# Kernel optimization log

Hardware: AMD Instinct MI355X
Metric: run time of the kernel (lower is better)

Reference implementation:

```python
import jax, jax.numpy as jnp
import numpy as np

B, C, CI, H, W = 8, 256, 128, 64, 64
EPS = 1e-5

def conv1x1(x, w, b):
    # x: [B,C,H,W], w: [O,C], b: [O]
    return jnp.einsum('bchw,oc->bohw', x, w) + b[None, :, None, None]

def avgpool2(x):
    b, c, h, w = x.shape
    return x.reshape(b, c, h // 2, 2, w // 2, 2).mean(axis=(3, 5))

def setup_inputs() -> dict:
    key = jax.random.key(0)
    ks = jax.random.split(key, 16)
    s = lambda fan: 1.0 / np.sqrt(fan)
    inp = {
        'q': jax.random.normal(ks[0], (B, C, H, W), jnp.float32),
        'k': jax.random.normal(ks[1], (B, C, H, W), jnp.float32),
        'v': jax.random.normal(ks[2], (B, C, H, W), jnp.float32),
        'Wg':  jax.random.normal(ks[3], (CI, C), jnp.float32) * s(C),
        'bg':  jax.random.normal(ks[4], (CI,), jnp.float32) * s(C),
        'Wth': jax.random.normal(ks[5], (CI, C), jnp.float32) * s(C),
        'bth': jax.random.normal(ks[6], (CI,), jnp.float32) * s(C),
        'Wph': jax.random.normal(ks[7], (CI, C), jnp.float32) * s(C),
        'bph': jax.random.normal(ks[8], (CI,), jnp.float32) * s(C),
        'Ww':  jax.random.normal(ks[9], (C, CI), jnp.float32) * s(CI),
        'bw':  jax.random.normal(ks[10], (C,), jnp.float32) * s(CI),
        'gamma': jax.random.normal(ks[11], (C,), jnp.float32) * 0.1 + 1.0,
        'beta':  jax.random.normal(ks[12], (C,), jnp.float32) * 0.1,
        'mean':  jax.random.normal(ks[13], (C,), jnp.float32) * 0.1,
        'var':   jax.random.uniform(ks[14], (C,), jnp.float32, 0.5, 1.5),
    }
    return inp

def reference(q, k, v, Wg, bg, Wth, bth, Wph, bph, Ww, bw, gamma, beta, mean, var):
    b = q.shape[0]
    # g branch on v, phi branch on q: 1x1 conv then 2x2 avg-pool (sub_sample)
    g_x = avgpool2(conv1x1(v, Wg, bg)).reshape(b, CI, -1)            # [B,CI,M]
    g_x = g_x.transpose(0, 2, 1)                                      # [B,M,CI]
    theta_x = conv1x1(k, Wth, bth).reshape(b, CI, -1).transpose(0, 2, 1)  # [B,N,CI]
    phi_x = avgpool2(conv1x1(q, Wph, bph)).reshape(b, CI, -1)        # [B,CI,M]
    f = jnp.einsum('bnc,bcm->bnm', theta_x, phi_x)                   # [B,N,M]
    f_div_C = jax.nn.softmax(f, axis=-1)
    y = jnp.einsum('bnm,bmc->bnc', f_div_C, g_x)                     # [B,N,CI]
    y = y.transpose(0, 2, 1).reshape(b, CI, H, W)
    W_y = conv1x1(y, Ww, bw)
    # BatchNorm2d (inference form)
    W_y = (W_y - mean[None, :, None, None]) * (gamma[None, :, None, None]
            * jax.lax.rsqrt(var + EPS)[None, :, None, None]) + beta[None, :, None, None]
    return W_y + v
```

## Files before the change

kernel.cpp:

```cpp
#include <hip/hip_runtime.h>
#include <cstddef>

typedef unsigned short u16;
typedef unsigned int u32;
typedef __attribute__((ext_vector_type(8))) __bf16 bf16x8;
typedef __attribute__((ext_vector_type(4))) float f32x4;

constexpr int kB = 8, kC = 256, kCI = 128, kN = 4096, kM = 1024;
constexpr int kCH = 64, kNCH = kM / kCH;
constexpr float kEPS = 1e-5f;
constexpr float kLOG2E = 1.44269504088896f;

__device__ __forceinline__ u16 f2bf(float f) {
    u32 u = __float_as_uint(f);
    u32 r = (u + 0x7fffu + ((u >> 16) & 1u)) >> 16;
    return (u16)r;
}

__device__ __forceinline__ void gload_lds16(const u16* g, u16* l) {
    __builtin_amdgcn_global_load_lds(
        (const __attribute__((address_space(1))) void*)g,
        (__attribute__((address_space(3))) void*)l, 16, 0, 0);
}

__global__ __launch_bounds__(256) void prep_kernel(const float* __restrict__ Wth,
                                                   const float* __restrict__ bth,
                                                   const float* __restrict__ Wph,
                                                   const float* __restrict__ Wg,
                                                   const float* __restrict__ Ww,
                                                   const float* __restrict__ bw,
                                                   const float* __restrict__ gamma,
                                                   const float* __restrict__ beta,
                                                   const float* __restrict__ mean,
                                                   const float* __restrict__ var,
                                                   u16* __restrict__ Wthb,
                                                   u16* __restrict__ Wphb,
                                                   u16* __restrict__ Wgb,
                                                   u16* __restrict__ Wwsb,
                                                   float* __restrict__ bb,
                                                   float* __restrict__ bthl) {
    int idx = blockIdx.x * 256 + threadIdx.x;
    if (idx < 32768) {
        Wthb[idx] = f2bf(Wth[idx] * kLOG2E);
        if (idx < kCI) bthl[idx] = bth[idx] * kLOG2E;
    } else if (idx < 65536) {
        int j = idx - 32768; Wphb[j] = f2bf(Wph[j]);
    } else if (idx < 98304) {
        int j = idx - 65536; Wgb[j] = f2bf(Wg[j]);
    } else {
        int j = idx - 98304;
        int co = j >> 7;
        float sc = gamma[co] * rsqrtf(var[co] + kEPS);
        Wwsb[j] = f2bf(Ww[j] * sc);
        if ((j & 127) == 0) bb[co] = (bw[co] - mean[co]) * sc + beta[co];
    }
}

template <int POOL>
__device__ __forceinline__ void conv_body(const float* __restrict__ x,
                                          const u16* __restrict__ Wb,
                                          const float* __restrict__ bias,
                                          u16* __restrict__ out, int Mn,
                                          int cmajor, int b, int n0,
                                          u16* x_lds) {
    int t = threadIdx.x;
    int w = t >> 6, lane = t & 63, l15 = lane & 15, quad = lane >> 4;
    int px = t & 63, cb8 = t >> 6;

    for (int cc8 = 0; cc8 < 8; cc8++) {
        int cb = cb8 * 8 + cc8;
        int c0 = cb * 8;
        float f[8];
        if (POOL) {
            int p = n0 + px, ph_ = p >> 5, pw_ = p & 31;
#pragma unroll
            for (int j = 0; j < 8; j++) {
                const float* src = x + ((size_t)(b * kC + c0 + j) * 64
                                        + 2 * ph_) * 64 + 2 * pw_;
                float2 a = *(const float2*)src;
                float2 b2 = *(const float2*)(src + 64);
                f[j] = 0.25f * (a.x + a.y + b2.x + b2.y);
            }
        } else {
#pragma unroll
            for (int j = 0; j < 8; j++)
                f[j] = x[(size_t)(b * kC + c0 + j) * Mn + n0 + px];
        }
        uint4 pk;
        pk.x = (u32)f2bf(f[0]) | ((u32)f2bf(f[1]) << 16);
        pk.y = (u32)f2bf(f[2]) | ((u32)f2bf(f[3]) << 16);
        pk.z = (u32)f2bf(f[4]) | ((u32)f2bf(f[5]) << 16);
        pk.w = (u32)f2bf(f[6]) | ((u32)f2bf(f[7]) << 16);
        *(uint4*)&x_lds[px * 256 + ((cb ^ (px & 7)) * 8)] = pk;
    }
    __syncthreads();

    f32x4 acc[8];
#pragma unroll
    for (int i = 0; i < 8; i++) acc[i] = (f32x4){0.f, 0.f, 0.f, 0.f};

    int rpx = w * 16 + l15;
#pragma unroll
    for (int ks = 0; ks < 8; ks++) {
        bf16x8 xf = *(const bf16x8*)&x_lds[rpx * 256 +
                                           (((ks * 4 + quad) ^ (rpx & 7)) * 8)];
#pragma unroll
        for (int ct = 0; ct < 8; ct++) {
            bf16x8 wf = *(const bf16x8*)&Wb[(ct * 16 + l15) * kC + ks * 32 + quad * 8];
            if (cmajor)
                acc[ct] = __builtin_amdgcn_mfma_f32_16x16x32_bf16(xf, wf, acc[ct], 0, 0, 0);
            else
                acc[ct] = __builtin_amdgcn_mfma_f32_16x16x32_bf16(wf, xf, acc[ct], 0, 0, 0);
        }
    }

    if (cmajor == 0) {
        int opx = n0 + w * 16 + l15;
#pragma unroll
        for (int ct = 0; ct < 8; ct++) {
            int ci0 = ct * 16 + quad * 4;
            uint2 pk;
            pk.x = (u32)f2bf(acc[ct][0] + bias[ci0 + 0]) |
                   ((u32)f2bf(acc[ct][1] + bias[ci0 + 1]) << 16);
            pk.y = (u32)f2bf(acc[ct][2] + bias[ci0 + 2]) |
                   ((u32)f2bf(acc[ct][3] + bias[ci0 + 3]) << 16);
            *(uint2*)&out[(size_t)(b * Mn + opx) * kCI + ci0] = pk;
        }
    } else {
        int opx = n0 + w * 16 + quad * 4;
#pragma unroll
        for (int ct = 0; ct < 8; ct++) {
            int ci = ct * 16 + l15;
            float bs = bias[ci];
            uint2 pk;
            pk.x = (u32)f2bf(acc[ct][0] + bs) | ((u32)f2bf(acc[ct][1] + bs) << 16);
            pk.y = (u32)f2bf(acc[ct][2] + bs) | ((u32)f2bf(acc[ct][3] + bs) << 16);
            *(uint2*)&out[(size_t)(b * kCI + ci) * Mn + opx] = pk;
        }
    }
}

__global__ __launch_bounds__(256, 4) void convs_kernel(const float* __restrict__ q,
                                                       const float* __restrict__ k,
                                                       const float* __restrict__ v,
                                                       const u16* __restrict__ Wthb,
                                                       const u16* __restrict__ Wphb,
                                                       const u16* __restrict__ Wgb,
                                                       const float* __restrict__ bthl,
                                                       const float* __restrict__ bph,
                                                       const float* __restrict__ bg,
                                                       u16* __restrict__ theta,
                                                       u16* __restrict__ phi,
                                                       u16* __restrict__ g) {
    __shared__ __align__(16) u16 x_lds[64 * 256];
    int bx = blockIdx.x, b = blockIdx.y;
    if (bx < 64) {
        conv_body<0>(k, Wthb, bthl, theta, kN, 0, b, bx * 64, x_lds);
    } else {
        int z = (bx >= 80);
        int n0 = (z ? (bx - 80) : (bx - 64)) * 64;
        conv_body<1>(z ? v : q, z ? Wgb : Wphb, z ? bg : bph, z ? g : phi,
                     kM, z, b, n0, x_lds);
    }
}

__global__ __launch_bounds__(256) void attn_kernel(const u16* __restrict__ theta,
                                                   const u16* __restrict__ phi,
                                                   const u16* __restrict__ g,
                                                   const u16* __restrict__ Wws,
                                                   const float* __restrict__ bb,
                                                   const float* __restrict__ v,
                                                   float* __restrict__ out) {
    __shared__ __align__(16) u16 ph_lds[2][8192];
    __shared__ __align__(16) u16 g_lds[2][8192];
    __shared__ __align__(16) u16 p_lds[4096];

    int t = threadIdx.x, b = blockIdx.y, n0 = blockIdx.x * 64;
    int w = t >> 6, lane = t & 63, l15 = lane & 15, quad = lane >> 4;
    int sw = (l15 >> 1) & 3;

    bf16x8 thf[4];
    const u16* thB = theta + ((size_t)(b * kN) + n0 + w * 16 + l15) * kCI;
#pragma unroll
    for (int ks = 0; ks < 4; ks++)
        thf[ks] = *(const bf16x8*)&thB[ks * 32 + quad * 8];

    f32x4 oacc[8];
#pragma unroll
    for (int ct = 0; ct < 8; ct++) oacc[ct] = (f32x4){0.f, 0.f, 0.f, 0.f};
    float m_ = -1e30f, l_ = 0.f;

    const u16* phB = phi + (size_t)b * kM * kCI;
    const u16* gB  = g   + (size_t)b * kCI * kM;
    u16* pw = p_lds + w * 1024;

    auto STAGE = [&](int buf, int ch) {
        int c0 = ch * kCH;
#pragma unroll
        for (int i = 0; i < 4; i++) {
            int W = t + 256 * i;
            int ks = W >> 8, m = (W >> 2) & 63, sl = W & 3;
            int cb = (ks << 2) | (sl ^ ((m >> 1) & 3));
            gload_lds16(phB + (size_t)(c0 + m) * kCI + cb * 8,
                        &ph_lds[buf][(w * 64 + i * 256) * 8]);
        }
#pragma unroll
        for (int i = 0; i < 4; i++) {
            int W = t + 256 * i;
            int ks2 = W >> 9, ci = (W >> 2) & 127, sl = W & 3;
            int mb = (ks2 << 2) | (sl ^ ((ci >> 1) & 3));
            gload_lds16(gB + (size_t)ci * kM + c0 + mb * 8,
                        &g_lds[buf][(w * 64 + i * 256) * 8]);
        }
    };

    STAGE(0, 0);

    for (int ch = 0; ch < kNCH; ++ch) {
        asm volatile("s_waitcnt vmcnt(0)" ::: "memory");
        __syncthreads();
        if (ch + 1 < kNCH) STAGE((ch + 1) & 1, ch + 1);
        const u16* phb = ph_lds[ch & 1];
        const u16* glb = g_lds[ch & 1];

        f32x4 sacc[4];
#pragma unroll
        for (int mt = 0; mt < 4; mt++) sacc[mt] = (f32x4){0.f, 0.f, 0.f, 0.f};
#pragma unroll
        for (int ks = 0; ks < 4; ks++)
#pragma unroll
            for (int mt = 0; mt < 4; mt++) {
                bf16x8 a = *(const bf16x8*)&phb[ks * 2048 + (mt * 16 + l15) * 32 +
                                                ((quad ^ sw) * 8)];
                sacc[mt] = __builtin_amdgcn_mfma_f32_16x16x32_bf16(a, thf[ks], sacc[mt], 0, 0, 0);
            }

        float mc = -1e30f;
#pragma unroll
        for (int mt = 0; mt < 4; mt++)
#pragma unroll
            for (int r = 0; r < 4; r++) mc = fmaxf(mc, sacc[mt][r]);
        mc = fmaxf(mc, __shfl_xor(mc, 16, 64));
        mc = fmaxf(mc, __shfl_xor(mc, 32, 64));
        if (__any(mc > m_ + 8.0f)) {
            float mn = fmaxf(m_, mc);
            float al = exp2f(m_ - mn);
            m_ = mn;
            l_ *= al;
#pragma unroll
            for (int ct = 0; ct < 8; ct++)
#pragma unroll
                for (int r = 0; r < 4; r++) oacc[ct][r] *= al;
        }
        float rs = 0.f;
#pragma unroll
        for (int mt = 0; mt < 4; mt++)
#pragma unroll
            for (int r = 0; r < 4; r++) {
                float p = exp2f(sacc[mt][r] - m_);
                sacc[mt][r] = p;
                rs += p;
            }
        l_ += rs;

#pragma unroll
        for (int mt = 0; mt < 4; mt++)
#pragma unroll
            for (int h = 0; h < 2; h++) {
                u32 d = (u32)f2bf(sacc[mt][2 * h]) | ((u32)f2bf(sacc[mt][2 * h + 1]) << 16);
                int m = mt * 16 + quad * 4 + 2 * h;
                int frag = m >> 5;
                int kblk = ((m >> 3) & 3);
                int j = (quad & 1) * 4 + 2 * h;
                *(u32*)&pw[frag * 512 + l15 * 32 + ((kblk ^ sw) * 8) + j] = d;
            }

#pragma unroll
        for (int ks2 = 0; ks2 < 2; ks2++) {
            bf16x8 bfrag = *(const bf16x8*)&pw[ks2 * 512 + l15 * 32 + ((quad ^ sw) * 8)];
#pragma unroll
            for (int ct = 0; ct < 8; ct++) {
                bf16x8 a = *(const bf16x8*)&glb[ks2 * 4096 + (ct * 16 + l15) * 32 +
                                                ((quad ^ sw) * 8)];
                oacc[ct] = __builtin_amdgcn_mfma_f32_16x16x32_bf16(a, bfrag, oacc[ct], 0, 0, 0);
            }
        }
    }

    l_ += __shfl_xor(l_, 16, 64);
    l_ += __shfl_xor(l_, 32, 64);
    float inv = 1.0f / l_;

    __syncthreads();
    u16* y_lds = &ph_lds[0][0];
    int nrow = w * 16 + l15;
#pragma unroll
    for (int ct = 0; ct < 8; ct++) {
        uint2 pk;
        pk.x = (u32)f2bf(oacc[ct][0] * inv) | ((u32)f2bf(oacc[ct][1] * inv) << 16);
        pk.y = (u32)f2bf(oacc[ct][2] * inv) | ((u32)f2bf(oacc[ct][3] * inv) << 16);
        *(uint2*)&y_lds[nrow * 136 + ct * 16 + quad * 4] = pk;
    }
    __syncthreads();

    bf16x8 af[4];
#pragma unroll
    for (int ks = 0; ks < 4; ks++)
        af[ks] = *(const bf16x8*)&y_lds[nrow * 136 + ks * 32 + quad * 8];

#pragma unroll
    for (int ct = 0; ct < 16; ct++) {
        int co = ct * 16 + l15;
        f32x4 a = (f32x4){0.f, 0.f, 0.f, 0.f};
#pragma unroll
        for (int ks = 0; ks < 4; ks++) {
            bf16x8 bf = *(const bf16x8*)&Wws[(size_t)co * kCI + ks * 32 + quad * 8];
            a = __builtin_amdgcn_mfma_f32_16x16x32_bf16(af[ks], bf, a, 0, 0, 0);
        }
        float bbv = bb[co];
        size_t base = (size_t)(b * kC + co) * kN + n0 + w * 16 + quad * 4;
        float4 vv = *(const float4*)&v[base];
        float4 ov;
        ov.x = a[0] + bbv + vv.x;
        ov.y = a[1] + bbv + vv.y;
        ov.z = a[2] + bbv + vv.z;
        ov.w = a[3] + bbv + vv.w;
        *(float4*)&out[base] = ov;
    }
}

extern "C" void kernel_launch(void* const* d_in, const int* in_sizes, int n_in,
                              void* d_out, int out_size, void* d_ws, size_t ws_size,
                              hipStream_t stream) {
    (void)in_sizes; (void)n_in; (void)out_size; (void)ws_size;
    const float* q     = (const float*)d_in[0];
    const float* k     = (const float*)d_in[1];
    const float* v     = (const float*)d_in[2];
    const float* Wg    = (const float*)d_in[3];
    const float* bg    = (const float*)d_in[4];
    const float* Wth   = (const float*)d_in[5];
    const float* bth   = (const float*)d_in[6];
    const float* Wph   = (const float*)d_in[7];
    const float* bph   = (const float*)d_in[8];
    const float* Ww    = (const float*)d_in[9];
    const float* bw    = (const float*)d_in[10];
    const float* gamma = (const float*)d_in[11];
    const float* beta  = (const float*)d_in[12];
    const float* mean  = (const float*)d_in[13];
    const float* var   = (const float*)d_in[14];
    float* out = (float*)d_out;

    u16* wsu = (u16*)d_ws;
    u16*   theta = wsu;
    u16*   phi   = theta + 4194304;
    u16*   gbuf  = phi + 1048576;
    u16*   Wthb  = gbuf + 1048576;
    u16*   Wphb  = Wthb + 32768;
    u16*   Wgb   = Wphb + 32768;
    u16*   Wwsb  = Wgb + 32768;
    float* bbuf  = (float*)(Wwsb + 32768);
    float* bthl  = bbuf + 256;

    prep_kernel<<<dim3(512), 256, 0, stream>>>(Wth, bth, Wph, Wg, Ww, bw, gamma, beta,
                                               mean, var, Wthb, Wphb, Wgb, Wwsb,
                                               bbuf, bthl);
    convs_kernel<<<dim3(96, 8), 256, 0, stream>>>(q, k, v, Wthb, Wphb, Wgb,
                                                  bthl, bph, bg, theta, phi, gbuf);
    attn_kernel<<<dim3(64, 8), 256, 0, stream>>>(theta, phi, gbuf, Wwsb, bbuf, v, out);
}
```

Measured before the change: 225.2 us.

## Fuse theta conv into attention kernel and split phi/g conv into smaller blocks

The theta 1x1 conv on k now runs inside the attention kernel's prologue. Each block converts its 64 pixels of k to bf16 in LDS, runs the MFMAs, and keeps the theta fragments in registers, so the 8 MB theta workspace is never written to or read back from global memory. The pooled phi/g convs move to their own kernel with 32-pixel tiles and a half-channel split per wave, giving 512 blocks instead of the previous 256 for that work. The cost is a longer attention prologue that reuses the phi/g LDS buffers with extra syncs, so the theta conv no longer overlaps with the other convs across the whole GPU.

```diff
diff --git a/kernel.cpp b/kernel.cpp
--- a/kernel.cpp
+++ b/kernel.cpp
@@ -56,35 +56,38 @@
     }
 }
 
-template <int POOL>
-__device__ __forceinline__ void conv_body(const float* __restrict__ x,
-                                          const u16* __restrict__ Wb,
-                                          const float* __restrict__ bias,
-                                          u16* __restrict__ out, int Mn,
-                                          int cmajor, int b, int n0,
-                                          u16* x_lds) {
+__global__ __launch_bounds__(256, 4) void convpg_kernel(const float* __restrict__ q,
+                                                        const float* __restrict__ v,
+                                                        const u16* __restrict__ Wphb,
+                                                        const u16* __restrict__ Wgb,
+                                                        const float* __restrict__ bph,
+                                                        const float* __restrict__ bg,
+                                                        u16* __restrict__ phi,
+                                                        u16* __restrict__ g) {
+    __shared__ __align__(16) u16 x_lds[32 * 256];
+    int z = blockIdx.z, b = blockIdx.y, n0 = blockIdx.x * 32;
+    const float* x = z ? v : q;
+    const u16* Wb = z ? Wgb : Wphb;
+    const float* bias = z ? bg : bph;
+    u16* outp = z ? g : phi;
+
     int t = threadIdx.x;
     int w = t >> 6, lane = t & 63, l15 = lane & 15, quad = lane >> 4;
-    int px = t & 63, cb8 = t >> 6;
-
-    for (int cc8 = 0; cc8 < 8; cc8++) {
-        int cb = cb8 * 8 + cc8;
+
+    int px = t & 31, cgrp = t >> 5;
+    int p = n0 + px, ph_ = p >> 5, pw_ = p & 31;
+#pragma unroll
+    for (int cc = 0; cc < 4; cc++) {
+        int cb = cgrp * 4 + cc;
         int c0 = cb * 8;
         float f[8];
-        if (POOL) {
-            int p = n0 + px, ph_ = p >> 5, pw_ = p & 31;
-#pragma unroll
-            for (int j = 0; j < 8; j++) {
-                const float* src = x + ((size_t)(b * kC + c0 + j) * 64
-                                        + 2 * ph_) * 64 + 2 * pw_;
-                float2 a = *(const float2*)src;
-                float2 b2 = *(const float2*)(src + 64);
-                f[j] = 0.25f * (a.x + a.y + b2.x + b2.y);
-            }
-        } else {
-#pragma unroll
-            for (int j = 0; j < 8; j++)
-                f[j] = x[(size_t)(b * kC + c0 + j) * Mn + n0 + px];
+#pragma unroll
+        for (int j = 0; j < 8; j++) {
+            const float* src = x + ((size_t)(b * kC + c0 + j) * 64 + 2 * ph_) * 64
+                               + 2 * pw_;
+            float2 a = *(const float2*)src;
+            float2 b2 = *(const float2*)(src + 64);
+            f[j] = 0.25f * (a.x + a.y + b2.x + b2.y);
         }
         uint4 pk;
         pk.x = (u32)f2bf(f[0]) | ((u32)f2bf(f[1]) << 16);
@@ -95,76 +98,56 @@
     }
     __syncthreads();
 
-    f32x4 acc[8];
-#pragma unroll
-    for (int i = 0; i < 8; i++) acc[i] = (f32x4){0.f, 0.f, 0.f, 0.f};
-
-    int rpx = w * 16 + l15;
+    int px_h = w >> 1, ci_h = w & 1;
+    f32x4 acc[4];
+#pragma unroll
+    for (int i = 0; i < 4; i++) acc[i] = (f32x4){0.f, 0.f, 0.f, 0.f};
+
+    int rpx = px_h * 16 + l15;
 #pragma unroll
     for (int ks = 0; ks < 8; ks++) {
         bf16x8 xf = *(const bf16x8*)&x_lds[rpx * 256 +
                                            (((ks * 4 + quad) ^ (rpx & 7)) * 8)];
 #pragma unroll
-        for (int ct = 0; ct < 8; ct++) {
-            bf16x8 wf = *(const bf16x8*)&Wb[(ct * 16 + l15) * kC + ks * 32 + quad * 8];
-            if (cmajor)
+        for (int ct = 0; ct < 4; ct++) {
+            int ci = ci_h * 64 + ct * 16 + l15;
+            bf16x8 wf = *(const bf16x8*)&Wb[ci * kC + ks * 32 + quad * 8];
+            if (z)
                 acc[ct] = __builtin_amdgcn_mfma_f32_16x16x32_bf16(xf, wf, acc[ct], 0, 0, 0);
             else
                 acc[ct] = __builtin_amdgcn_mfma_f32_16x16x32_bf16(wf, xf, acc[ct], 0, 0, 0);
         }
     }
 
-    if (cmajor == 0) {
-        int opx = n0 + w * 16 + l15;
-#pragma unroll
-        for (int ct = 0; ct < 8; ct++) {
-            int ci0 = ct * 16 + quad * 4;
+    if (!z) {
+        int opx = n0 + px_h * 16 + l15;
+#pragma unroll
+        for (int ct = 0; ct < 4; ct++) {
+            int ci0 = ci_h * 64 + ct * 16 + quad * 4;
             uint2 pk;
             pk.x = (u32)f2bf(acc[ct][0] + bias[ci0 + 0]) |
                    ((u32)f2bf(acc[ct][1] + bias[ci0 + 1]) << 16);
             pk.y = (u32)f2bf(acc[ct][2] + bias[ci0 + 2]) |
                    ((u32)f2bf(acc[ct][3] + bias[ci0 + 3]) << 16);
-            *(uint2*)&out[(size_t)(b * Mn + opx) * kCI + ci0] = pk;
+            *(uint2*)&outp[(size_t)(b * kM + opx) * kCI + ci0] = pk;
         }
     } else {
-        int opx = n0 + w * 16 + quad * 4;
-#pragma unroll
-        for (int ct = 0; ct < 8; ct++) {
-            int ci = ct * 16 + l15;
+        int opx = n0 + px_h * 16 + quad * 4;
+#pragma unroll
+        for (int ct = 0; ct < 4; ct++) {
+            int ci = ci_h * 64 + ct * 16 + l15;
             float bs = bias[ci];
             uint2 pk;
             pk.x = (u32)f2bf(acc[ct][0] + bs) | ((u32)f2bf(acc[ct][1] + bs) << 16);
             pk.y = (u32)f2bf(acc[ct][2] + bs) | ((u32)f2bf(acc[ct][3] + bs) << 16);
-            *(uint2*)&out[(size_t)(b * kCI + ci) * Mn + opx] = pk;
-        }
-    }
-}
-
-__global__ __launch_bounds__(256, 4) void convs_kernel(const float* __restrict__ q,
-                                                       const float* __restrict__ k,
-                                                       const float* __restrict__ v,
-                                                       const u16* __restrict__ Wthb,
-                                                       const u16* __restrict__ Wphb,
-                                                       const u16* __restrict__ Wgb,
-                                                       const float* __restrict__ bthl,
-                                                       const float* __restrict__ bph,
-                                                       const float* __restrict__ bg,
-                                                       u16* __restrict__ theta,
-                                                       u16* __restrict__ phi,
-                                                       u16* __restrict__ g) {
-    __shared__ __align__(16) u16 x_lds[64 * 256];
-    int bx = blockIdx.x, b = blockIdx.y;
-    if (bx < 64) {
-        conv_body<0>(k, Wthb, bthl, theta, kN, 0, b, bx * 64, x_lds);
-    } else {
-        int z = (bx >= 80);
-        int n0 = (z ? (bx - 80) : (bx - 64)) * 64;
-        conv_body<1>(z ? v : q, z ? Wgb : Wphb, z ? bg : bph, z ? g : phi,
-                     kM, z, b, n0, x_lds);
-    }
-}
-
-__global__ __launch_bounds__(256) void attn_kernel(const u16* __restrict__ theta,
+            *(uint2*)&outp[(size_t)(b * kCI + ci) * kM + opx] = pk;
+        }
+    }
+}
+
+__global__ __launch_bounds__(256) void attn_kernel(const float* __restrict__ k,
+                                                   const u16* __restrict__ Wthb,
+                                                   const float* __restrict__ bthl,
                                                    const u16* __restrict__ phi,
                                                    const u16* __restrict__ g,
                                                    const u16* __restrict__ Wws,
@@ -180,10 +163,55 @@
     int sw = (l15 >> 1) & 3;
 
     bf16x8 thf[4];
-    const u16* thB = theta + ((size_t)(b * kN) + n0 + w * 16 + l15) * kCI;
-#pragma unroll
-    for (int ks = 0; ks < 4; ks++)
-        thf[ks] = *(const bf16x8*)&thB[ks * 32 + quad * 8];
+    {
+        u16* x_lds = &ph_lds[0][0];
+        u16* th_lds = &g_lds[0][0];
+        int px = t & 63, cb8 = t >> 6;
+        for (int cc8 = 0; cc8 < 8; cc8++) {
+            int cb = cb8 * 8 + cc8;
+            int c0 = cb * 8;
+            float f[8];
+#pragma unroll
+            for (int j = 0; j < 8; j++)
+                f[j] = k[(size_t)(b * kC + c0 + j) * kN + n0 + px];
+            uint4 pk;
+            pk.x = (u32)f2bf(f[0]) | ((u32)f2bf(f[1]) << 16);
+            pk.y = (u32)f2bf(f[2]) | ((u32)f2bf(f[3]) << 16);
+            pk.z = (u32)f2bf(f[4]) | ((u32)f2bf(f[5]) << 16);
+            pk.w = (u32)f2bf(f[6]) | ((u32)f2bf(f[7]) << 16);
+            *(uint4*)&x_lds[px * 256 + ((cb ^ (px & 7)) * 8)] = pk;
+        }
+        __syncthreads();
+
+        f32x4 acc[8];
+#pragma unroll
+        for (int i = 0; i < 8; i++) acc[i] = (f32x4){0.f, 0.f, 0.f, 0.f};
+        int rpx = w * 16 + l15;
+#pragma unroll
+        for (int ks = 0; ks < 8; ks++) {
+            bf16x8 xf = *(const bf16x8*)&x_lds[rpx * 256 +
+                                               (((ks * 4 + quad) ^ (rpx & 7)) * 8)];
+#pragma unroll
+            for (int ct = 0; ct < 8; ct++) {
+                bf16x8 wf = *(const bf16x8*)&Wthb[(ct * 16 + l15) * kC + ks * 32 + quad * 8];
+                acc[ct] = __builtin_amdgcn_mfma_f32_16x16x32_bf16(wf, xf, acc[ct], 0, 0, 0);
+            }
+        }
+#pragma unroll
+        for (int ct = 0; ct < 8; ct++) {
+            int ci0 = ct * 16 + quad * 4;
+            uint2 pk;
+            pk.x = (u32)f2bf(acc[ct][0] + bthl[ci0 + 0]) |
+                   ((u32)f2bf(acc[ct][1] + bthl[ci0 + 1]) << 16);
+            pk.y = (u32)f2bf(acc[ct][2] + bthl[ci0 + 2]) |
+                   ((u32)f2bf(acc[ct][3] + bthl[ci0 + 3]) << 16);
+            *(uint2*)&th_lds[rpx * 136 + ci0] = pk;
+        }
+#pragma unroll
+        for (int ks = 0; ks < 4; ks++)
+            thf[ks] = *(const bf16x8*)&th_lds[rpx * 136 + ks * 32 + quad * 8];
+        __syncthreads();
+    }
 
     f32x4 oacc[8];
 #pragma unroll
@@ -351,8 +379,7 @@
     float* out = (float*)d_out;
 
     u16* wsu = (u16*)d_ws;
-    u16*   theta = wsu;
-    u16*   phi   = theta + 4194304;
+    u16*   phi   = wsu;
     u16*   gbuf  = phi + 1048576;
     u16*   Wthb  = gbuf + 1048576;
     u16*   Wphb  = Wthb + 32768;
@@ -364,7 +391,8 @@
     prep_kernel<<<dim3(512), 256, 0, stream>>>(Wth, bth, Wph, Wg, Ww, bw, gamma, beta,
                                                mean, var, Wthb, Wphb, Wgb, Wwsb,
                                                bbuf, bthl);
-    convs_kernel<<<dim3(96, 8), 256, 0, stream>>>(q, k, v, Wthb, Wphb, Wgb,
-                                                  bthl, bph, bg, theta, phi, gbuf);
-    attn_kernel<<<dim3(64, 8), 256, 0, stream>>>(theta, phi, gbuf, Wwsb, bbuf, v, out);
-}
+    convpg_kernel<<<dim3(32, 8, 2), 256, 0, stream>>>(q, v, Wphb, Wgb, bph, bg,
+                                                      phi, gbuf);
+    attn_kernel<<<dim3(64, 8), 256, 0, stream>>>(k, Wthb, bthl, phi, gbuf,
+                                                 Wwsb, bbuf, v, out);
+}
```

Measured after the change: 232.8 us. 1.03x slower.

## Split attention key dimension across two wave groups and merge softmax states

Applied to the files above, without the earlier changes.

The attention block grows to 512 threads, and the two groups of four waves each process half of the 1024 keys with 32-key chunks. The partial accumulators and max/sum statistics are merged through LDS in a flash-decoding-style combine. The output projection is then split across the groups by output channel. This raises per-CU wave parallelism on a grid of only 512 blocks, at the cost of an extra LDS exchange, more barriers and smaller per-chunk MFMA batches.

```diff
diff --git a/kernel.cpp b/kernel.cpp
--- a/kernel.cpp
+++ b/kernel.cpp
@@ -7,7 +7,9 @@
 typedef __attribute__((ext_vector_type(4))) float f32x4;
 
 constexpr int kB = 8, kC = 256, kCI = 128, kN = 4096, kM = 1024;
-constexpr int kCH = 64, kNCH = kM / kCH;
+constexpr int kHM = 512;
+constexpr int kCH = 32;
+constexpr int kNCH = kHM / kCH;
 constexpr float kEPS = 1e-5f;
 constexpr float kLOG2E = 1.44269504088896f;
 
@@ -164,23 +166,25 @@
     }
 }
 
-__global__ __launch_bounds__(256) void attn_kernel(const u16* __restrict__ theta,
-                                                   const u16* __restrict__ phi,
-                                                   const u16* __restrict__ g,
-                                                   const u16* __restrict__ Wws,
-                                                   const float* __restrict__ bb,
-                                                   const float* __restrict__ v,
-                                                   float* __restrict__ out) {
-    __shared__ __align__(16) u16 ph_lds[2][8192];
-    __shared__ __align__(16) u16 g_lds[2][8192];
-    __shared__ __align__(16) u16 p_lds[4096];
+__global__ __launch_bounds__(512, 4) void attn_kernel(const u16* __restrict__ theta,
+                                                      const u16* __restrict__ phi,
+                                                      const u16* __restrict__ g,
+                                                      const u16* __restrict__ Wws,
+                                                      const float* __restrict__ bb,
+                                                      const float* __restrict__ v,
+                                                      float* __restrict__ out) {
+    __shared__ __align__(16) u16 ph_lds[2][2][4096];
+    __shared__ __align__(16) u16 g_lds[2][2][4096];
+    __shared__ __align__(16) u16 p_lds[8 * 512];
+    __shared__ float mlsh[128];
 
     int t = threadIdx.x, b = blockIdx.y, n0 = blockIdx.x * 64;
     int w = t >> 6, lane = t & 63, l15 = lane & 15, quad = lane >> 4;
+    int grp = w >> 2, wl = w & 3, th = t & 255;
     int sw = (l15 >> 1) & 3;
 
     bf16x8 thf[4];
-    const u16* thB = theta + ((size_t)(b * kN) + n0 + w * 16 + l15) * kCI;
+    const u16* thB = theta + ((size_t)(b * kN) + n0 + wl * 16 + l15) * kCI;
 #pragma unroll
     for (int ks = 0; ks < 4; ks++)
         thf[ks] = *(const bf16x8*)&thB[ks * 32 + quad * 8];
@@ -192,25 +196,25 @@
 
     const u16* phB = phi + (size_t)b * kM * kCI;
     const u16* gB  = g   + (size_t)b * kCI * kM;
-    u16* pw = p_lds + w * 1024;
+    u16* pw = p_lds + w * 512;
 
     auto STAGE = [&](int buf, int ch) {
-        int c0 = ch * kCH;
-#pragma unroll
-        for (int i = 0; i < 4; i++) {
-            int W = t + 256 * i;
-            int ks = W >> 8, m = (W >> 2) & 63, sl = W & 3;
+        int c0 = grp * kHM + ch * kCH;
+#pragma unroll
+        for (int i = 0; i < 2; i++) {
+            int W = th + 256 * i;
+            int ks = W >> 7, m = (W >> 2) & 31, sl = W & 3;
             int cb = (ks << 2) | (sl ^ ((m >> 1) & 3));
             gload_lds16(phB + (size_t)(c0 + m) * kCI + cb * 8,
-                        &ph_lds[buf][(w * 64 + i * 256) * 8]);
-        }
-#pragma unroll
-        for (int i = 0; i < 4; i++) {
-            int W = t + 256 * i;
-            int ks2 = W >> 9, ci = (W >> 2) & 127, sl = W & 3;
-            int mb = (ks2 << 2) | (sl ^ ((ci >> 1) & 3));
+                        &ph_lds[grp][buf][(wl * 64 + i * 256) * 8]);
+        }
+#pragma unroll
+        for (int i = 0; i < 2; i++) {
+            int W = th + 256 * i;
+            int ci = W >> 2, sl = W & 3;
+            int mb = sl ^ ((ci >> 1) & 3);
             gload_lds16(gB + (size_t)ci * kM + c0 + mb * 8,
-                        &g_lds[buf][(w * 64 + i * 256) * 8]);
+                        &g_lds[grp][buf][(wl * 64 + i * 256) * 8]);
         }
     };
 
@@ -220,24 +224,24 @@
         asm volatile("s_waitcnt vmcnt(0)" ::: "memory");
         __syncthreads();
         if (ch + 1 < kNCH) STAGE((ch + 1) & 1, ch + 1);
-        const u16* phb = ph_lds[ch & 1];
-        const u16* glb = g_lds[ch & 1];
-
-        f32x4 sacc[4];
-#pragma unroll
-        for (int mt = 0; mt < 4; mt++) sacc[mt] = (f32x4){0.f, 0.f, 0.f, 0.f};
+        const u16* phb = ph_lds[grp][ch & 1];
+        const u16* glb = g_lds[grp][ch & 1];
+
+        f32x4 sacc[2];
+#pragma unroll
+        for (int mt = 0; mt < 2; mt++) sacc[mt] = (f32x4){0.f, 0.f, 0.f, 0.f};
 #pragma unroll
         for (int ks = 0; ks < 4; ks++)
 #pragma unroll
-            for (int mt = 0; mt < 4; mt++) {
-                bf16x8 a = *(const bf16x8*)&phb[ks * 2048 + (mt * 16 + l15) * 32 +
+            for (int mt = 0; mt < 2; mt++) {
+                bf16x8 a = *(const bf16x8*)&phb[ks * 1024 + (mt * 16 + l15) * 32 +
                                                 ((quad ^ sw) * 8)];
                 sacc[mt] = __builtin_amdgcn_mfma_f32_16x16x32_bf16(a, thf[ks], sacc[mt], 0, 0, 0);
             }
 
         float mc = -1e30f;
 #pragma unroll
-        for (int mt = 0; mt < 4; mt++)
+        for (int mt = 0; mt < 2; mt++)
 #pragma unroll
             for (int r = 0; r < 4; r++) mc = fmaxf(mc, sacc[mt][r]);
         mc = fmaxf(mc, __shfl_xor(mc, 16, 64));
@@ -254,7 +258,7 @@
         }
         float rs = 0.f;
 #pragma unroll
-        for (int mt = 0; mt < 4; mt++)
+        for (int mt = 0; mt < 2; mt++)
 #pragma unroll
             for (int r = 0; r < 4; r++) {
                 float p = exp2f(sacc[mt][r] - m_);
@@ -264,53 +268,68 @@
         l_ += rs;
 
 #pragma unroll
-        for (int mt = 0; mt < 4; mt++)
+        for (int mt = 0; mt < 2; mt++)
 #pragma unroll
             for (int h = 0; h < 2; h++) {
                 u32 d = (u32)f2bf(sacc[mt][2 * h]) | ((u32)f2bf(sacc[mt][2 * h + 1]) << 16);
                 int m = mt * 16 + quad * 4 + 2 * h;
-                int frag = m >> 5;
-                int kblk = ((m >> 3) & 3);
+                int kblk = (m >> 3) & 3;
                 int j = (quad & 1) * 4 + 2 * h;
-                *(u32*)&pw[frag * 512 + l15 * 32 + ((kblk ^ sw) * 8) + j] = d;
+                *(u32*)&pw[l15 * 32 + ((kblk ^ sw) * 8) + j] = d;
             }
 
-#pragma unroll
-        for (int ks2 = 0; ks2 < 2; ks2++) {
-            bf16x8 bfrag = *(const bf16x8*)&pw[ks2 * 512 + l15 * 32 + ((quad ^ sw) * 8)];
-#pragma unroll
-            for (int ct = 0; ct < 8; ct++) {
-                bf16x8 a = *(const bf16x8*)&glb[ks2 * 4096 + (ct * 16 + l15) * 32 +
-                                                ((quad ^ sw) * 8)];
-                oacc[ct] = __builtin_amdgcn_mfma_f32_16x16x32_bf16(a, bfrag, oacc[ct], 0, 0, 0);
-            }
+        bf16x8 bfrag = *(const bf16x8*)&pw[l15 * 32 + ((quad ^ sw) * 8)];
+#pragma unroll
+        for (int ct = 0; ct < 8; ct++) {
+            bf16x8 a = *(const bf16x8*)&glb[(ct * 16 + l15) * 32 + ((quad ^ sw) * 8)];
+            oacc[ct] = __builtin_amdgcn_mfma_f32_16x16x32_bf16(a, bfrag, oacc[ct], 0, 0, 0);
         }
     }
 
     l_ += __shfl_xor(l_, 16, 64);
     l_ += __shfl_xor(l_, 32, 64);
-    float inv = 1.0f / l_;
 
     __syncthreads();
-    u16* y_lds = &ph_lds[0][0];
-    int nrow = w * 16 + l15;
+    float* olds = (float*)&ph_lds[0][0][0];
+    u16* y_lds = &g_lds[0][0][0];
+    int nl = wl * 16 + l15;
+    if (grp == 1) {
+#pragma unroll
+        for (int ct = 0; ct < 8; ct++) {
+            int s = (ct * 4 + quad) ^ (nl & 7);
+            *(f32x4*)&olds[nl * 128 + s * 4] = oacc[ct];
+        }
+        if (quad == 0) { mlsh[2 * nl] = m_; mlsh[2 * nl + 1] = l_; }
+    }
+    __syncthreads();
+    if (grp == 0) {
+        float m1 = mlsh[2 * nl], l1 = mlsh[2 * nl + 1];
+        float mm = fmaxf(m_, m1);
+        float w0 = exp2f(m_ - mm), w1 = exp2f(m1 - mm);
+        float inv = 1.0f / (l_ * w0 + l1 * w1);
+        float a0 = w0 * inv, a1 = w1 * inv;
+#pragma unroll
+        for (int ct = 0; ct < 8; ct++) {
+            int s = (ct * 4 + quad) ^ (nl & 7);
+            f32x4 o1 = *(const f32x4*)&olds[nl * 128 + s * 4];
+            uint2 pk;
+            pk.x = (u32)f2bf(oacc[ct][0] * a0 + o1[0] * a1) |
+                   ((u32)f2bf(oacc[ct][1] * a0 + o1[1] * a1) << 16);
+            pk.y = (u32)f2bf(oacc[ct][2] * a0 + o1[2] * a1) |
+                   ((u32)f2bf(oacc[ct][3] * a0 + o1[3] * a1) << 16);
+            *(uint2*)&y_lds[nl * 136 + ct * 16 + quad * 4] = pk;
+        }
+    }
+    __syncthreads();
+
+    bf16x8 af[4];
+#pragma unroll
+    for (int ks = 0; ks < 4; ks++)
+        af[ks] = *(const bf16x8*)&y_lds[nl * 136 + ks * 32 + quad * 8];
+
 #pragma unroll
     for (int ct = 0; ct < 8; ct++) {
-        uint2 pk;
-        pk.x = (u32)f2bf(oacc[ct][0] * inv) | ((u32)f2bf(oacc[ct][1] * inv) << 16);
-        pk.y = (u32)f2bf(oacc[ct][2] * inv) | ((u32)f2bf(oacc[ct][3] * inv) << 16);
-        *(uint2*)&y_lds[nrow * 136 + ct * 16 + quad * 4] = pk;
-    }
-    __syncthreads();
-
-    bf16x8 af[4];
-#pragma unroll
-    for (int ks = 0; ks < 4; ks++)
-        af[ks] = *(const bf16x8*)&y_lds[nrow * 136 + ks * 32 + quad * 8];
-
-#pragma unroll
-    for (int ct = 0; ct < 16; ct++) {
-        int co = ct * 16 + l15;
+        int co = grp * 128 + ct * 16 + l15;
         f32x4 a = (f32x4){0.f, 0.f, 0.f, 0.f};
 #pragma unroll
         for (int ks = 0; ks < 4; ks++) {
@@ -318,7 +337,7 @@
             a = __builtin_amdgcn_mfma_f32_16x16x32_bf16(af[ks], bf, a, 0, 0, 0);
         }
         float bbv = bb[co];
-        size_t base = (size_t)(b * kC + co) * kN + n0 + w * 16 + quad * 4;
+        size_t base = (size_t)(b * kC + co) * kN + n0 + wl * 16 + quad * 4;
         float4 vv = *(const float4*)&v[base];
         float4 ov;
         ov.x = a[0] + bbv + vv.x;
@@ -366,5 +385,5 @@
                                                bbuf, bthl);
     convs_kernel<<<dim3(96, 8), 256, 0, stream>>>(q, k, v, Wthb, Wphb, Wgb,
                                                   bthl, bph, bg, theta, phi, gbuf);
-    attn_kernel<<<dim3(64, 8), 256, 0, stream>>>(theta, phi, gbuf, Wwsb, bbuf, v, out);
-}
+    attn_kernel<<<dim3(64, 8), 512, 0, stream>>>(theta, phi, gbuf, Wwsb, bbuf, v, out);
+}
```

Measured after the change: 220.7 us. 1.02x faster.
